# Optimization experiments

Measured on AMD Instinct MI355X. Metric: run time of the kernel, lower is better.

## Reference

```python
import jax, jax.numpy as jnp
import numpy as np

F_DIM = 32          # phi_feature_dim
P = 128             # preselection_ap (spatial H=W)
NU = 4              # num_users
N1 = NU - 1         # n_cat1 == n_cat2
N3 = (NU - 1) ** 2  # n_cat3


def setup_inputs() -> dict:
    key = jax.random.key(0)
    k1, k2, k3, k4, k5 = jax.random.split(key, 5)
    B, CIN = 32, 8
    phi_input = jax.random.normal(k1, (B, CIN, P, P), dtype=jnp.float32)
    W1 = jax.random.normal(k2, (4 * F_DIM, CIN), dtype=jnp.float32) * 0.1
    b1 = jax.random.normal(k3, (4 * F_DIM,), dtype=jnp.float32) * 0.1
    W3 = jax.random.normal(k4, (4 * F_DIM, 4 * F_DIM), dtype=jnp.float32) * 0.1
    b3 = jax.random.normal(k5, (4 * F_DIM,), dtype=jnp.float32) * 0.1
    ex = jnp.ones((P, P), dtype=jnp.float32) - jnp.eye(P, dtype=jnp.float32)
    return {"phi_input": phi_input, "W1": W1, "b1": b1, "W3": W3, "b3": b3, "ex": ex}


def _conv1x1(x, W, b):
    # 1x1 conv == channel matmul: [b,c,h,w] x [o,c] -> [b,o,h,w]
    return jnp.einsum('bchw,oc->bohw', x, W) + b[None, :, None, None]


def _postprocess(r, ex):
    f = F_DIM
    c0 = r[:, :f]
    c1 = jnp.einsum('ph,bchw->bcpw', ex, r[:, f:2 * f]) / N1
    c2 = jnp.einsum('bchw,wq->bchq', r[:, 2 * f:3 * f], ex) / N1
    c3 = jnp.einsum('ph,bchw,wq->bcpq', ex, r[:, 3 * f:4 * f], ex) / N3
    return jnp.concatenate((c0, c1, c2, c3), axis=1)


def reference(phi_input, W1, b1, W3, b3, ex):
    r = jax.nn.relu(_conv1x1(phi_input, W1, b1))
    r = _postprocess(r, ex)
    r = jax.nn.relu(_conv1x1(r, W3, b3))
    r = _postprocess(r, ex)
    return r
```

## Files before the change

### kernel.cpp

```cpp
#include <hip/hip_runtime.h>
#include <stdint.h>

#define BATCH 32
#define CIN   8
#define NCH   128
#define PP    128
#define VCH   96

typedef __attribute__((ext_vector_type(8))) short    bf16x8;
typedef __attribute__((ext_vector_type(4))) float    f32x4;

__device__ __forceinline__ float bf2f(unsigned short u) {
    union { unsigned int i; float f; } x; x.i = ((unsigned int)u) << 16; return x.f;
}
__device__ __forceinline__ unsigned short f2bf(float f) {
    union { float f; unsigned int i; } x; x.f = f;
    unsigned int r = x.i + 0x7fffu + ((x.i >> 16) & 1u);
    return (unsigned short)(r >> 16);
}

#define SWZB(row, cb) (((row) << 8) + ((cb) ^ (((row) & 7) << 4)))

__global__ __launch_bounds__(512) void k1_sums(const float* __restrict__ phi,
        const float* __restrict__ W1, const float* __restrict__ b1,
        float* __restrict__ RS1t, float* __restrict__ CS1) {
    __shared__ float S[17408];
    float* phi_s   = S;
    float* cs_full = S;
    float* rs_part = S + 16896;
    int bx = blockIdx.x;
    int b = bx >> 4, strip = bx & 15;
    int p0 = strip * 8;
    int tid = threadIdx.x;
    int c = tid & 127, qq = tid >> 7;

    for (int k = tid; k < 8192; k += 512) {
        int pi = k >> 10, ci = (k >> 7) & 7, q = k & 127;
        phi_s[k] = phi[((b * CIN + ci) * PP + p0 + pi) * PP + q];
    }
    float4 w1a = *(const float4*)(W1 + c * 8);
    float4 w1b = *(const float4*)(W1 + c * 8 + 4);
    float b1c = b1[c];
    float cs_acc[32];
    #pragma unroll
    for (int j = 0; j < 32; ++j) cs_acc[j] = 0.f;
    __syncthreads();

    for (int pi = 0; pi < 8; ++pi) {
        float rsp = 0.f;
        const float* pb = phi_s + pi * 1024;
        #pragma unroll
        for (int j4 = 0; j4 < 8; ++j4) {
            int q4 = qq * 32 + j4 * 4;
            float4 ph[8];
            #pragma unroll
            for (int ci = 0; ci < 8; ++ci)
                ph[ci] = *(const float4*)(pb + ci * 128 + q4);
            #pragma unroll
            for (int e = 0; e < 4; ++e) {
                float t = b1c;
                t = fmaf(w1a.x, ((const float*)&ph[0])[e], t);
                t = fmaf(w1a.y, ((const float*)&ph[1])[e], t);
                t = fmaf(w1a.z, ((const float*)&ph[2])[e], t);
                t = fmaf(w1a.w, ((const float*)&ph[3])[e], t);
                t = fmaf(w1b.x, ((const float*)&ph[4])[e], t);
                t = fmaf(w1b.y, ((const float*)&ph[5])[e], t);
                t = fmaf(w1b.z, ((const float*)&ph[6])[e], t);
                t = fmaf(w1b.w, ((const float*)&ph[7])[e], t);
                t = fmaxf(t, 0.f);
                cs_acc[j4 * 4 + e] += t;
                rsp += t;
            }
        }
        rs_part[c * 4 + qq] = rsp;
        __syncthreads();
        if (tid < 128) {
            float4 r4 = *(const float4*)(rs_part + tid * 4);
            RS1t[(b * PP + p0 + pi) * NCH + tid] = r4.x + r4.y + r4.z + r4.w;
        }
        __syncthreads();
    }
    #pragma unroll
    for (int j4 = 0; j4 < 8; ++j4) {
        float4 v = {cs_acc[j4 * 4], cs_acc[j4 * 4 + 1], cs_acc[j4 * 4 + 2], cs_acc[j4 * 4 + 3]};
        *(float4*)(cs_full + c * 132 + qq * 32 + j4 * 4) = v;
    }
    __syncthreads();
    for (int k = tid; k < 16384; k += 512) {
        int cc = k >> 7, q = k & 127;
        atomicAdd(&CS1[(b * NCH + cc) * PP + q], cs_full[cc * 132 + q]);
    }
}

__global__ __launch_bounds__(256) void k1b_planes(const float* __restrict__ W3,
        const float* __restrict__ b3, const float* __restrict__ RS1t,
        const float* __restrict__ CS1, float* __restrict__ Ap,
        float* __restrict__ Bq, float* __restrict__ Cc,
        unsigned short* __restrict__ W3bf) {
    int b = blockIdx.x, tid = threadIdx.x;
    __shared__ float s1_l[128];
    __shared__ float cs_g[64][132];
    __shared__ float rs_g[64][132];
    if (tid < 128) {
        float s = 0.f;
        for (int p = 0; p < 128; ++p) s += RS1t[(b * PP + p) * NCH + tid];
        s1_l[tid] = s;
    }
    for (int k = tid; k < 64 * 128; k += 256) {
        int r = k >> 7, q = k & 127;
        int ch_c = (r < 32) ? (32 + r) : (64 + r);
        cs_g[r][q] = CS1[(b * NCH + ch_c) * PP + q];
    }
    for (int k = tid; k < 64 * 128; k += 256) {
        int p = k >> 6, r = k & 63;
        rs_g[r][p] = RS1t[(b * PP + p) * NCH + 64 + r];
    }
    __syncthreads();
    int o = tid >> 1, qh = tid & 1;
    {
        float wa[64];
        #pragma unroll
        for (int r = 0; r < 64; ++r)
            wa[r] = (r < 32) ? W3[o * NCH + 32 + r] * (1.f / 3.f)
                             : -W3[o * NCH + 64 + r] * (1.f / 9.f);
        for (int jq = 0; jq < 16; ++jq) {
            int q = qh * 64 + jq * 4;
            float4 a = {0.f, 0.f, 0.f, 0.f};
            #pragma unroll
            for (int r = 0; r < 64; ++r) {
                float4 cv = *(const float4*)&cs_g[r][q];
                a.x = fmaf(wa[r], cv.x, a.x);
                a.y = fmaf(wa[r], cv.y, a.y);
                a.z = fmaf(wa[r], cv.z, a.z);
                a.w = fmaf(wa[r], cv.w, a.w);
            }
            *(float4*)&Ap[(b * NCH + o) * PP + q] = a;
        }
    }
    {
        float wb[64];
        #pragma unroll
        for (int r = 0; r < 64; ++r)
            wb[r] = (r < 32) ? W3[o * NCH + 64 + r] * (1.f / 3.f)
                             : -W3[o * NCH + 64 + r] * (1.f / 9.f);
        for (int jp = 0; jp < 16; ++jp) {
            int p = qh * 64 + jp * 4;
            float4 a = {0.f, 0.f, 0.f, 0.f};
            #pragma unroll
            for (int r = 0; r < 64; ++r) {
                float4 rv = *(const float4*)&rs_g[r][p];
                a.x = fmaf(wb[r], rv.x, a.x);
                a.y = fmaf(wb[r], rv.y, a.y);
                a.z = fmaf(wb[r], rv.z, a.z);
                a.w = fmaf(wb[r], rv.w, a.w);
            }
            *(float4*)&Bq[(b * NCH + o) * PP + p] = a;
        }
    }
    if (tid < 128) {
        float cv = b3[tid];
        #pragma unroll
        for (int r = 0; r < 32; ++r)
            cv = fmaf(W3[tid * NCH + 96 + r] * (1.f / 9.f), s1_l[96 + r], cv);
        Cc[b * NCH + tid] = cv;
    }
    if (b == 0) {
        for (int i = 0; i < 16; ++i) {
            int k = tid + i * 256;
            float4 w = *(const float4*)(W3 + k * 4);
            int c0 = (k * 4) & 127;
            float sc = (c0 < 32) ? 1.f : ((c0 < 96) ? (-1.f / 3.f) : (1.f / 9.f));
            unsigned int lo = (unsigned int)f2bf(w.x * sc) | ((unsigned int)f2bf(w.y * sc) << 16);
            unsigned int hi = (unsigned int)f2bf(w.z * sc) | ((unsigned int)f2bf(w.w * sc) << 16);
            uint2 u = {lo, hi};
            *(uint2*)(W3bf + k * 4) = u;
        }
    }
}

__global__ __launch_bounds__(256) void k2_mfma(const float* __restrict__ phi,
        const float* __restrict__ W1, const float* __restrict__ b1,
        const unsigned short* __restrict__ W3bf,
        const float* __restrict__ Ap, const float* __restrict__ Bq,
        const float* __restrict__ Cc, float* __restrict__ out,
        unsigned short* __restrict__ v2) {
    int b = blockIdx.x >> 7, p = blockIdx.x & 127;
    __shared__ unsigned short w3_l[16384];
    __shared__ unsigned short t_l[16384];
    __shared__ float phi_l[8][128];
    __shared__ float BC_l[128];
    int tid = threadIdx.x;

    #pragma unroll
    for (int i = 0; i < 8; ++i) {
        int k = tid + i * 256;
        int o = k >> 4, cb = (k & 15) * 16;
        bf16x8 v = *(const bf16x8*)(W3bf + k * 8);
        *(bf16x8*)((char*)w3_l + SWZB(o, cb)) = v;
    }
    for (int k = tid; k < 1024; k += 256) {
        int ci = k >> 7, q = k & 127;
        phi_l[ci][q] = phi[((b * CIN + ci) * PP + p) * PP + q];
    }
    if (tid < 128) BC_l[tid] = Bq[(b * NCH + tid) * PP + p] + Cc[b * NCH + tid];
    __syncthreads();

    int c_t = tid & 127;
    int pg  = tid >> 7;
    float4 w1a = *(const float4*)(W1 + c_t * 8);
    float4 w1b = *(const float4*)(W1 + c_t * 8 + 4);
    float b1t = b1[c_t];
    #pragma unroll 4
    for (int i4 = 0; i4 < 16; ++i4) {
        int pix = pg * 64 + i4 * 4;
        float4 ph[8];
        #pragma unroll
        for (int ci = 0; ci < 8; ++ci)
            ph[ci] = *(const float4*)&phi_l[ci][pix];
        #pragma unroll
        for (int e = 0; e < 4; ++e) {
            float t = b1t;
            t = fmaf(w1a.x, ((const float*)&ph[0])[e], t);
            t = fmaf(w1a.y, ((const float*)&ph[1])[e], t);
            t = fmaf(w1a.z, ((const float*)&ph[2])[e], t);
            t = fmaf(w1a.w, ((const float*)&ph[3])[e], t);
            t = fmaf(w1b.x, ((const float*)&ph[4])[e], t);
            t = fmaf(w1b.y, ((const float*)&ph[5])[e], t);
            t = fmaf(w1b.z, ((const float*)&ph[6])[e], t);
            t = fmaf(w1b.w, ((const float*)&ph[7])[e], t);
            *(unsigned short*)((char*)t_l + SWZB(pix + e, c_t * 2)) = f2bf(fmaxf(t, 0.f));
        }
    }
    __syncthreads();

    int wv = tid >> 6, l = tid & 63;
    int lr = l & 15, lg = l >> 4;
    bf16x8 afr[2][4];
    #pragma unroll
    for (int m = 0; m < 2; ++m) {
        int q = (wv * 2 + m) * 16 + lr;
        #pragma unroll
        for (int ks = 0; ks < 4; ++ks)
            afr[m][ks] = *(const bf16x8*)((char*)t_l + SWZB(q, ks * 64 + lg * 16));
    }
    f32x4 acc[2][8];
    #pragma unroll
    for (int nt = 0; nt < 8; ++nt) {
        int o = nt * 16 + lr;
        float bc = BC_l[o];
        #pragma unroll
        for (int m = 0; m < 2; ++m) {
            int q0 = (wv * 2 + m) * 16 + lg * 4;
            f32x4 ap = *(const f32x4*)(Ap + ((size_t)(b * NCH + o)) * PP + q0);
            acc[m][nt] = ap + bc;
        }
    }
    #pragma unroll
    for (int nt = 0; nt < 8; ++nt) {
        int o = nt * 16 + lr;
        bf16x8 bfr[4];
        #pragma unroll
        for (int ks = 0; ks < 4; ++ks)
            bfr[ks] = *(const bf16x8*)((char*)w3_l + SWZB(o, ks * 64 + lg * 16));
        #pragma unroll
        for (int m = 0; m < 2; ++m)
            #pragma unroll
            for (int ks = 0; ks < 4; ++ks)
                acc[m][nt] = __builtin_amdgcn_mfma_f32_16x16x32_bf16(
                                 afr[m][ks], bfr[ks], acc[m][nt], 0, 0, 0);
    }
    __syncthreads();
    unsigned short* v_l = t_l;
    #pragma unroll
    for (int nt = 0; nt < 2; ++nt) {
        int o = nt * 16 + lr;
        #pragma unroll
        for (int m = 0; m < 2; ++m) {
            int q0 = (wv * 2 + m) * 16 + lg * 4;
            f32x4 a = acc[m][nt];
            f32x4 r = {fmaxf(a.x, 0.f), fmaxf(a.y, 0.f), fmaxf(a.z, 0.f), fmaxf(a.w, 0.f)};
            *(f32x4*)(out + ((size_t)((b * NCH + o) * PP + p)) * PP + q0) = r;
        }
    }
    #pragma unroll
    for (int m = 0; m < 2; ++m) {
        int q0 = (wv * 2 + m) * 16 + lg * 4;
        #pragma unroll
        for (int nt = 2; nt < 8; ++nt) {
            int o = nt * 16 + lr;
            f32x4 a = acc[m][nt];
            unsigned int lo = (unsigned int)f2bf(fmaxf(a.x, 0.f))
                            | ((unsigned int)f2bf(fmaxf(a.y, 0.f)) << 16);
            unsigned int hi = (unsigned int)f2bf(fmaxf(a.z, 0.f))
                            | ((unsigned int)f2bf(fmaxf(a.w, 0.f)) << 16);
            uint2 u = {lo, hi};
            *(uint2*)((char*)v_l + SWZB(o, q0 * 2)) = u;
        }
    }
    __syncthreads();
    #pragma unroll
    for (int i = 0; i < 6; ++i) {
        int k = tid + i * 256;
        int o = 32 + (k >> 4), j = k & 15;
        bf16x8 v = *(const bf16x8*)((char*)v_l + SWZB(o, j * 16));
        *(bf16x8*)(v2 + ((size_t)(b * VCH + (o - 32)) * PP + p) * PP + j * 8) = v;
    }
}

__global__ __launch_bounds__(256) void k3_out(const unsigned short* __restrict__ v2,
        float* __restrict__ out) {
    int bx = blockIdx.x;
    int b = bx / VCH, cr = bx - b * VCH;
    int ch = 32 + cr;
    int g = ch >> 5;
    __shared__ float rsp[128][16];
    __shared__ float csp[16][128];
    __shared__ float rs_l[128], cs_l[128];
    __shared__ float s_sh;
    int tid = threadIdx.x;
    const unsigned short* src = v2 + (size_t)(b * VCH + cr) * (PP * PP);

    int pc = tid >> 4, qc = tid & 15;
    float cs8[8];
    #pragma unroll
    for (int e = 0; e < 8; ++e) cs8[e] = 0.f;
    #pragma unroll
    for (int i = 0; i < 8; ++i) {
        int pr = pc * 8 + i;
        bf16x8 u = *(const bf16x8*)(src + pr * PP + qc * 8);
        float rp = 0.f;
        #pragma unroll
        for (int e = 0; e < 8; ++e) {
            float v = bf2f((unsigned short)u[e]);
            cs8[e] += v;
            rp += v;
        }
        rsp[pr][qc] = rp;
    }
    f32x4 clo = {cs8[0], cs8[1], cs8[2], cs8[3]};
    f32x4 chi = {cs8[4], cs8[5], cs8[6], cs8[7]};
    *(f32x4*)&csp[pc][qc * 8]     = clo;
    *(f32x4*)&csp[pc][qc * 8 + 4] = chi;
    __syncthreads();
    if (tid < 128) {
        f32x4 a = *(const f32x4*)&rsp[tid][0];
        f32x4 c2 = *(const f32x4*)&rsp[tid][4];
        f32x4 c3 = *(const f32x4*)&rsp[tid][8];
        f32x4 c4 = *(const f32x4*)&rsp[tid][12];
        rs_l[tid] = (a.x + a.y + a.z + a.w) + (c2.x + c2.y + c2.z + c2.w)
                  + (c3.x + c3.y + c3.z + c3.w) + (c4.x + c4.y + c4.z + c4.w);
    } else {
        int q = tid - 128;
        float s = 0.f;
        #pragma unroll
        for (int i = 0; i < 16; ++i) s += csp[i][q];
        cs_l[q] = s;
    }
    __syncthreads();
    if (tid < 64) {
        float s = rs_l[tid] + rs_l[tid + 64];
        #pragma unroll
        for (int off = 32; off > 0; off >>= 1) s += __shfl_down(s, off);
        if (tid == 0) s_sh = s;
    }
    __syncthreads();
    float stot = s_sh;

    float* dst = out + (size_t)(b * NCH + ch) * (PP * PP);
    #pragma unroll
    for (int i = 0; i < 8; ++i) {
        int k = tid + i * 256;
        int pr = k >> 4, q0 = (k & 15) * 8;
        bf16x8 u = *(const bf16x8*)(src + pr * PP + q0);
        float rp = rs_l[pr];
        float o8[8];
        #pragma unroll
        for (int e = 0; e < 8; ++e) {
            float v = bf2f((unsigned short)u[e]);
            float cq = cs_l[q0 + e];
            float r;
            if (g == 1)      r = (cq - v) * (1.f / 3.f);
            else if (g == 2) r = (rp - v) * (1.f / 3.f);
            else             r = (stot - rp - cq + v) * (1.f / 9.f);
            o8[e] = r;
        }
        f32x4 lo = {o8[0], o8[1], o8[2], o8[3]};
        f32x4 hi = {o8[4], o8[5], o8[6], o8[7]};
        *(f32x4*)(dst + pr * PP + q0)     = lo;
        *(f32x4*)(dst + pr * PP + q0 + 4) = hi;
    }
}

extern "C" void kernel_launch(void* const* d_in, const int* in_sizes, int n_in,
                              void* d_out, int out_size, void* d_ws, size_t ws_size,
                              hipStream_t stream) {
    (void)in_sizes; (void)n_in; (void)out_size; (void)ws_size;
    const float* phi = (const float*)d_in[0];
    const float* W1  = (const float*)d_in[1];
    const float* b1  = (const float*)d_in[2];
    const float* W3  = (const float*)d_in[3];
    const float* b3  = (const float*)d_in[4];
    float* out = (float*)d_out;

    char* ws = (char*)d_ws;
    unsigned short* v2 = (unsigned short*)ws;
    size_t off = (size_t)BATCH * VCH * PP * PP * 2;
    float* RS1t = (float*)(ws + off); off += (size_t)BATCH * NCH * PP * 4;
    float* CS1  = (float*)(ws + off); off += (size_t)BATCH * NCH * PP * 4;
    float* Ap   = (float*)(ws + off); off += (size_t)BATCH * NCH * PP * 4;
    float* Bq   = (float*)(ws + off); off += (size_t)BATCH * NCH * PP * 4;
    float* Cc   = (float*)(ws + off); off += (size_t)BATCH * NCH * 4;
    unsigned short* W3bf = (unsigned short*)(ws + off); off += (size_t)NCH * NCH * 2;

    hipMemsetAsync(CS1, 0, (size_t)BATCH * NCH * PP * 4, stream);
    k1_sums<<<BATCH * 16, 512, 0, stream>>>(phi, W1, b1, RS1t, CS1);
    k1b_planes<<<BATCH, 256, 0, stream>>>(W3, b3, RS1t, CS1, Ap, Bq, Cc, W3bf);
    k2_mfma<<<BATCH * PP, 256, 0, stream>>>(phi, W1, b1, W3bf, Ap, Bq, Cc, out, v2);
    k3_out<<<BATCH * VCH, 256, 0, stream>>>(v2, out);
}
```

Measured before the change: 232.1 us.

## Use MFMA for first conv, replace atomics with strip partials, widen k1b grid

In k2, the first 1x1 conv now runs as a bf16 MFMA with K padded to 32 instead of scalar FP32 FMAs. Phi and W1 are converted to bf16 in LDS and the bias is used as the accumulator init. k1_sums now writes per-strip column-sum partials (8 strips of 16 rows) instead of atomics, which removes the memset. k1b_planes sums those partials and splits each batch across 4 blocks by output-channel group, raising its parallelism from 32 blocks. These changes add bf16 rounding of the first conv inputs and extra partial-buffer traffic.

```diff
diff --git a/kernel.cpp b/kernel.cpp
--- a/kernel.cpp
+++ b/kernel.cpp
@@ -6,6 +6,7 @@
 #define NCH   128
 #define PP    128
 #define VCH   96
+#define NSTRIP 8
 
 typedef __attribute__((ext_vector_type(8))) short    bf16x8;
 typedef __attribute__((ext_vector_type(4))) float    f32x4;
@@ -23,18 +24,18 @@
 
 __global__ __launch_bounds__(512) void k1_sums(const float* __restrict__ phi,
         const float* __restrict__ W1, const float* __restrict__ b1,
-        float* __restrict__ RS1t, float* __restrict__ CS1) {
+        float* __restrict__ RS1t, float* __restrict__ CS1p) {
     __shared__ float S[17408];
     float* phi_s   = S;
     float* cs_full = S;
     float* rs_part = S + 16896;
     int bx = blockIdx.x;
-    int b = bx >> 4, strip = bx & 15;
-    int p0 = strip * 8;
+    int b = bx >> 3, strip = bx & 7;
+    int p0 = strip * 16;
     int tid = threadIdx.x;
     int c = tid & 127, qq = tid >> 7;
 
-    for (int k = tid; k < 8192; k += 512) {
+    for (int k = tid; k < 16384; k += 512) {
         int pi = k >> 10, ci = (k >> 7) & 7, q = k & 127;
         phi_s[k] = phi[((b * CIN + ci) * PP + p0 + pi) * PP + q];
     }
@@ -46,7 +47,7 @@
     for (int j = 0; j < 32; ++j) cs_acc[j] = 0.f;
     __syncthreads();
 
-    for (int pi = 0; pi < 8; ++pi) {
+    for (int pi = 0; pi < 16; ++pi) {
         float rsp = 0.f;
         const float* pb = phi_s + pi * 1024;
         #pragma unroll
@@ -86,45 +87,53 @@
         *(float4*)(cs_full + c * 132 + qq * 32 + j4 * 4) = v;
     }
     __syncthreads();
+    float* dstp = CS1p + (size_t)(b * NSTRIP + strip) * NCH * PP;
     for (int k = tid; k < 16384; k += 512) {
         int cc = k >> 7, q = k & 127;
-        atomicAdd(&CS1[(b * NCH + cc) * PP + q], cs_full[cc * 132 + q]);
+        dstp[k] = cs_full[cc * 132 + q];
     }
 }
 
 __global__ __launch_bounds__(256) void k1b_planes(const float* __restrict__ W3,
         const float* __restrict__ b3, const float* __restrict__ RS1t,
-        const float* __restrict__ CS1, float* __restrict__ Ap,
+        const float* __restrict__ CS1p, float* __restrict__ Ap,
         float* __restrict__ Bq, float* __restrict__ Cc,
         unsigned short* __restrict__ W3bf) {
-    int b = blockIdx.x, tid = threadIdx.x;
-    __shared__ float s1_l[128];
+    int bx = blockIdx.x;
+    int b = bx >> 2, og = bx & 3;
+    int tid = threadIdx.x;
     __shared__ float cs_g[64][132];
     __shared__ float rs_g[64][132];
-    if (tid < 128) {
-        float s = 0.f;
-        for (int p = 0; p < 128; ++p) s += RS1t[(b * PP + p) * NCH + tid];
-        s1_l[tid] = s;
-    }
+    __shared__ float s1_96[32];
     for (int k = tid; k < 64 * 128; k += 256) {
         int r = k >> 7, q = k & 127;
         int ch_c = (r < 32) ? (32 + r) : (64 + r);
-        cs_g[r][q] = CS1[(b * NCH + ch_c) * PP + q];
+        float s = 0.f;
+        #pragma unroll
+        for (int s8 = 0; s8 < NSTRIP; ++s8)
+            s += CS1p[((size_t)(b * NSTRIP + s8) * NCH + ch_c) * PP + q];
+        cs_g[r][q] = s;
     }
     for (int k = tid; k < 64 * 128; k += 256) {
         int p = k >> 6, r = k & 63;
         rs_g[r][p] = RS1t[(b * PP + p) * NCH + 64 + r];
     }
     __syncthreads();
-    int o = tid >> 1, qh = tid & 1;
+    if (og == 0 && tid < 32) {
+        float s = 0.f;
+        for (int q = 0; q < 128; ++q) s += cs_g[32 + tid][q];
+        s1_96[tid] = s;
+    }
+    int o = og * 32 + (tid >> 3), qh = tid & 7;
     {
         float wa[64];
         #pragma unroll
         for (int r = 0; r < 64; ++r)
             wa[r] = (r < 32) ? W3[o * NCH + 32 + r] * (1.f / 3.f)
                              : -W3[o * NCH + 64 + r] * (1.f / 9.f);
-        for (int jq = 0; jq < 16; ++jq) {
-            int q = qh * 64 + jq * 4;
+        #pragma unroll
+        for (int j = 0; j < 4; ++j) {
+            int q = qh * 16 + j * 4;
             float4 a = {0.f, 0.f, 0.f, 0.f};
             #pragma unroll
             for (int r = 0; r < 64; ++r) {
@@ -143,8 +152,9 @@
         for (int r = 0; r < 64; ++r)
             wb[r] = (r < 32) ? W3[o * NCH + 64 + r] * (1.f / 3.f)
                              : -W3[o * NCH + 64 + r] * (1.f / 9.f);
-        for (int jp = 0; jp < 16; ++jp) {
-            int p = qh * 64 + jp * 4;
+        #pragma unroll
+        for (int j = 0; j < 4; ++j) {
+            int p = qh * 16 + j * 4;
             float4 a = {0.f, 0.f, 0.f, 0.f};
             #pragma unroll
             for (int r = 0; r < 64; ++r) {
@@ -157,14 +167,15 @@
             *(float4*)&Bq[(b * NCH + o) * PP + p] = a;
         }
     }
-    if (tid < 128) {
+    __syncthreads();
+    if (og == 0 && tid < 128) {
         float cv = b3[tid];
         #pragma unroll
         for (int r = 0; r < 32; ++r)
-            cv = fmaf(W3[tid * NCH + 96 + r] * (1.f / 9.f), s1_l[96 + r], cv);
+            cv = fmaf(W3[tid * NCH + 96 + r] * (1.f / 9.f), s1_96[r], cv);
         Cc[b * NCH + tid] = cv;
     }
-    if (b == 0) {
+    if (bx == 0) {
         for (int i = 0; i < 16; ++i) {
             int k = tid + i * 256;
             float4 w = *(const float4*)(W3 + k * 4);
@@ -187,10 +198,16 @@
     int b = blockIdx.x >> 7, p = blockIdx.x & 127;
     __shared__ unsigned short w3_l[16384];
     __shared__ unsigned short t_l[16384];
-    __shared__ float phi_l[8][128];
+    __shared__ unsigned short phi_b[128 * 36];
+    __shared__ unsigned short w1_b[128 * 36];
     __shared__ float BC_l[128];
+    __shared__ float b1_l[128];
     int tid = threadIdx.x;
 
+    for (int k = tid; k < 2304; k += 256) {
+        ((unsigned int*)phi_b)[k] = 0u;
+        ((unsigned int*)w1_b)[k] = 0u;
+    }
     #pragma unroll
     for (int i = 0; i < 8; ++i) {
         int k = tid + i * 256;
@@ -198,43 +215,64 @@
         bf16x8 v = *(const bf16x8*)(W3bf + k * 8);
         *(bf16x8*)((char*)w3_l + SWZB(o, cb)) = v;
     }
-    for (int k = tid; k < 1024; k += 256) {
-        int ci = k >> 7, q = k & 127;
-        phi_l[ci][q] = phi[((b * CIN + ci) * PP + p) * PP + q];
-    }
-    if (tid < 128) BC_l[tid] = Bq[(b * NCH + tid) * PP + p] + Cc[b * NCH + tid];
-    __syncthreads();
-
-    int c_t = tid & 127;
-    int pg  = tid >> 7;
-    float4 w1a = *(const float4*)(W1 + c_t * 8);
-    float4 w1b = *(const float4*)(W1 + c_t * 8 + 4);
-    float b1t = b1[c_t];
-    #pragma unroll 4
-    for (int i4 = 0; i4 < 16; ++i4) {
-        int pix = pg * 64 + i4 * 4;
-        float4 ph[8];
-        #pragma unroll
-        for (int ci = 0; ci < 8; ++ci)
-            ph[ci] = *(const float4*)&phi_l[ci][pix];
-        #pragma unroll
-        for (int e = 0; e < 4; ++e) {
-            float t = b1t;
-            t = fmaf(w1a.x, ((const float*)&ph[0])[e], t);
-            t = fmaf(w1a.y, ((const float*)&ph[1])[e], t);
-            t = fmaf(w1a.z, ((const float*)&ph[2])[e], t);
-            t = fmaf(w1a.w, ((const float*)&ph[3])[e], t);
-            t = fmaf(w1b.x, ((const float*)&ph[4])[e], t);
-            t = fmaf(w1b.y, ((const float*)&ph[5])[e], t);
-            t = fmaf(w1b.z, ((const float*)&ph[6])[e], t);
-            t = fmaf(w1b.w, ((const float*)&ph[7])[e], t);
-            *(unsigned short*)((char*)t_l + SWZB(pix + e, c_t * 2)) = f2bf(fmaxf(t, 0.f));
-        }
+    if (tid < 128) {
+        BC_l[tid] = Bq[(b * NCH + tid) * PP + p] + Cc[b * NCH + tid];
+        b1_l[tid] = b1[tid];
+    }
+    __syncthreads();
+    {
+        int idx = tid * 4;
+        int ci = idx >> 7, q0 = idx & 127;
+        float4 v = *(const float4*)(phi + ((size_t)(b * CIN + ci) * PP + p) * PP + q0);
+        phi_b[(q0 + 0) * 36 + ci] = f2bf(v.x);
+        phi_b[(q0 + 1) * 36 + ci] = f2bf(v.y);
+        phi_b[(q0 + 2) * 36 + ci] = f2bf(v.z);
+        phi_b[(q0 + 3) * 36 + ci] = f2bf(v.w);
+    }
+    {
+        int idx = tid * 4;
+        int c = idx >> 3, k0 = idx & 7;
+        float4 v = *(const float4*)(W1 + c * 8 + k0);
+        w1_b[c * 36 + k0 + 0] = f2bf(v.x);
+        w1_b[c * 36 + k0 + 1] = f2bf(v.y);
+        w1_b[c * 36 + k0 + 2] = f2bf(v.z);
+        w1_b[c * 36 + k0 + 3] = f2bf(v.w);
     }
     __syncthreads();
 
     int wv = tid >> 6, l = tid & 63;
     int lr = l & 15, lg = l >> 4;
+
+    {
+        bf16x8 afr1[2];
+        f32x4 binit[2];
+        #pragma unroll
+        for (int i = 0; i < 2; ++i) {
+            int ct = wv * 2 + i;
+            afr1[i] = *(const bf16x8*)((char*)w1_b + (ct * 16 + lr) * 72 + lg * 16);
+            int c0 = ct * 16 + lg * 4;
+            f32x4 bi = {b1_l[c0], b1_l[c0 + 1], b1_l[c0 + 2], b1_l[c0 + 3]};
+            binit[i] = bi;
+        }
+        #pragma unroll
+        for (int pt = 0; pt < 8; ++pt) {
+            int pix = pt * 16 + lr;
+            bf16x8 bfr1 = *(const bf16x8*)((char*)phi_b + pix * 72 + lg * 16);
+            #pragma unroll
+            for (int i = 0; i < 2; ++i) {
+                int c0 = (wv * 2 + i) * 16 + lg * 4;
+                f32x4 a = __builtin_amdgcn_mfma_f32_16x16x32_bf16(afr1[i], bfr1, binit[i], 0, 0, 0);
+                unsigned int lo = (unsigned int)f2bf(fmaxf(a.x, 0.f))
+                                | ((unsigned int)f2bf(fmaxf(a.y, 0.f)) << 16);
+                unsigned int hi = (unsigned int)f2bf(fmaxf(a.z, 0.f))
+                                | ((unsigned int)f2bf(fmaxf(a.w, 0.f)) << 16);
+                uint2 u = {lo, hi};
+                *(uint2*)((char*)t_l + SWZB(pix, c0 * 2)) = u;
+            }
+        }
+    }
+    __syncthreads();
+
     bf16x8 afr[2][4];
     #pragma unroll
     for (int m = 0; m < 2; ++m) {
@@ -343,7 +381,7 @@
     *(f32x4*)&csp[pc][qc * 8 + 4] = chi;
     __syncthreads();
     if (tid < 128) {
-        f32x4 a = *(const f32x4*)&rsp[tid][0];
+        f32x4 a  = *(const f32x4*)&rsp[tid][0];
         f32x4 c2 = *(const f32x4*)&rsp[tid][4];
         f32x4 c3 = *(const f32x4*)&rsp[tid][8];
         f32x4 c4 = *(const f32x4*)&rsp[tid][12];
@@ -406,15 +444,14 @@
     unsigned short* v2 = (unsigned short*)ws;
     size_t off = (size_t)BATCH * VCH * PP * PP * 2;
     float* RS1t = (float*)(ws + off); off += (size_t)BATCH * NCH * PP * 4;
-    float* CS1  = (float*)(ws + off); off += (size_t)BATCH * NCH * PP * 4;
+    float* CS1p = (float*)(ws + off); off += (size_t)BATCH * NSTRIP * NCH * PP * 4;
     float* Ap   = (float*)(ws + off); off += (size_t)BATCH * NCH * PP * 4;
     float* Bq   = (float*)(ws + off); off += (size_t)BATCH * NCH * PP * 4;
     float* Cc   = (float*)(ws + off); off += (size_t)BATCH * NCH * 4;
     unsigned short* W3bf = (unsigned short*)(ws + off); off += (size_t)NCH * NCH * 2;
 
-    hipMemsetAsync(CS1, 0, (size_t)BATCH * NCH * PP * 4, stream);
-    k1_sums<<<BATCH * 16, 512, 0, stream>>>(phi, W1, b1, RS1t, CS1);
-    k1b_planes<<<BATCH, 256, 0, stream>>>(W3, b3, RS1t, CS1, Ap, Bq, Cc, W3bf);
+    k1_sums<<<BATCH * NSTRIP, 512, 0, stream>>>(phi, W1, b1, RS1t, CS1p);
+    k1b_planes<<<BATCH * 4, 256, 0, stream>>>(W3, b3, RS1t, CS1p, Ap, Bq, Cc, W3bf);
     k2_mfma<<<BATCH * PP, 256, 0, stream>>>(phi, W1, b1, W3bf, Ap, Bq, Cc, out, v2);
     k3_out<<<BATCH * VCH, 256, 0, stream>>>(v2, out);
 }
```

Result: faster. 224.5 us (-3.3%).
